# Optimization experiments

Measured on AMD Instinct MI355X. Metric: run time of the kernel, lower is better.

## Reference

```python
import jax, jax.numpy as jnp
import numpy as np
from jax import lax

H = 32   # hidden_size
L = 8    # num_layers
D_IN = 64    # lstm input_size / fc0 out
FEAT = 4096  # feature_size
T = 300      # frame_size
B = 64       # batch


def setup_inputs() -> dict:
    key = jax.random.key(0)
    ks = jax.random.split(key, 16)
    s = 0.05
    inp = {
        "x": jax.random.normal(ks[0], (B, T, FEAT), dtype=jnp.float32),
        # fc0: Linear(4096->64), ReLU, Dropout(eval), Linear(64->64)
        "W0": jax.random.normal(ks[1], (D_IN, FEAT), dtype=jnp.float32) * s,
        "b0": jax.random.normal(ks[2], (D_IN,), dtype=jnp.float32) * s,
        "W1": jax.random.normal(ks[3], (D_IN, D_IN), dtype=jnp.float32) * s,
        "b1": jax.random.normal(ks[4], (D_IN,), dtype=jnp.float32) * s,
        # LSTM params, PyTorch layout: W_ih [4H, in], W_hh [4H, H], biases [4H]
        "Wih0": jax.random.normal(ks[5], (4 * H, D_IN), dtype=jnp.float32) * s,
        "Wih": jax.random.normal(ks[6], (L - 1, 4 * H, H), dtype=jnp.float32) * s,
        "Whh": jax.random.normal(ks[7], (L, 4 * H, H), dtype=jnp.float32) * s,
        "bih": jax.random.normal(ks[8], (L, 4 * H), dtype=jnp.float32) * s,
        "bhh": jax.random.normal(ks[9], (L, 4 * H), dtype=jnp.float32) * s,
        # fc1: 32 -> 1 ; fc2: 300 -> 1
        "Wfc1": jax.random.normal(ks[10], (1, H), dtype=jnp.float32) * s,
        "bfc1": jax.random.normal(ks[11], (1,), dtype=jnp.float32) * s,
        "Wfc2": jax.random.normal(ks[12], (1, T), dtype=jnp.float32) * s,
        "bfc2": jax.random.normal(ks[13], (1,), dtype=jnp.float32) * s,
    }
    return inp


def _lstm_layer(x_seq, Wih_l, Whh_l, bih_l, bhh_l):
    # x_seq: [B, T, in] -> h_seq: [B, T, H]; PyTorch gate order i,f,g,o
    gx = jnp.einsum('bti,gi->btg', x_seq, Wih_l) + bih_l  # [B,T,4H]
    b = x_seq.shape[0]
    init = (jnp.zeros((b, H), x_seq.dtype), jnp.zeros((b, H), x_seq.dtype))

    def step(carry, gx_t):
        h, c = carry
        g = gx_t + h @ Whh_l.T + bhh_l
        i, f, gg, o = jnp.split(g, 4, axis=-1)
        c = jax.nn.sigmoid(f) * c + jax.nn.sigmoid(i) * jnp.tanh(gg)
        h = jax.nn.sigmoid(o) * jnp.tanh(c)
        return (h, c), h

    _, hs = lax.scan(step, init, jnp.swapaxes(gx, 0, 1))  # hs: [T,B,H]
    return jnp.swapaxes(hs, 0, 1)


def reference(x, W0, b0, W1, b1, Wih0, Wih, Whh, bih, bhh, Wfc1, bfc1, Wfc2, bfc2):
    # fc0 (dropout is identity in eval mode)
    h = jax.nn.relu(jnp.einsum('btf,of->bto', x, W0) + b0)
    h = jnp.einsum('bti,oi->bto', h, W1) + b1  # [B,T,64]
    # stacked LSTM, h0=c0=0
    for l in range(L):
        Wih_l = Wih0 if l == 0 else Wih[l - 1]
        h = _lstm_layer(h, Wih_l, Whh[l], bih[l], bhh[l])  # [B,T,32]
    # fc1 over hidden, squeeze, fc2 over time, squeeze
    y = jnp.einsum('bth,oh->bto', h, Wfc1)[..., 0] + bfc1[0]  # [B,T]
    y = y @ Wfc2.T + bfc2  # [B,1]
    return y[:, 0]
```

## Files before the change

kernel.cpp:

```cpp
#include <hip/hip_runtime.h>
#include <cstdint>

#define FEAT 4096
#define DIN  64
#define HS   32
#define NL   8
#define TT   300
#define BB   64
#define G4   128
#define MROWS (BB*TT)
#define KS    4
#define KSLICE (FEAT/KS)
#define BK    64
#define NCHUNK (KSLICE/BK)

typedef __bf16 bf16x8 __attribute__((ext_vector_type(8)));
typedef float  f32x4  __attribute__((ext_vector_type(4)));
typedef unsigned short u16x8 __attribute__((ext_vector_type(8)));

__device__ __forceinline__ float sigm(float x){ return __fdividef(1.f, 1.f + __expf(-x)); }
__device__ __forceinline__ float tanh_f(float x){ return __fdividef(2.f, 1.f + __expf(-2.f*x)) - 1.f; }

__device__ __forceinline__ unsigned short bf16_rne(float f){
    uint32_t u = __float_as_uint(f);
    return (unsigned short)((u + 0x7FFFu + ((u >> 16) & 1u)) >> 16);
}

__global__ __launch_bounds__(256) void w0split(const float* __restrict__ W0,
                                               unsigned short* __restrict__ wh,
                                               unsigned short* __restrict__ wl)
{
    const int i = (blockIdx.x * 256 + threadIdx.x) * 4;
    float4 v = *(const float4*)(W0 + i);
    float f[4] = {v.x, v.y, v.z, v.w};
    unsigned short hh[4], ll[4];
    #pragma unroll
    for (int j = 0; j < 4; ++j) {
        unsigned short h = bf16_rne(f[j]);
        float fh = __uint_as_float((uint32_t)h << 16);
        hh[j] = h;
        ll[j] = bf16_rne(f[j] - fh);
    }
    *(ushort4*)(wh + i) = make_ushort4(hh[0], hh[1], hh[2], hh[3]);
    *(ushort4*)(wl + i) = make_ushort4(ll[0], ll[1], ll[2], ll[3]);
}

__global__ __launch_bounds__(256, 2) void fc_gemm1(
    const float* __restrict__ x,
    const unsigned short* __restrict__ wh,
    const unsigned short* __restrict__ wl,
    float* __restrict__ part)
{
    __shared__ __align__(16) unsigned short xh[2][64][64];
    __shared__ __align__(16) unsigned short xl[2][64][64];
    __shared__ __align__(16) unsigned short wh_s[2][64][64];
    __shared__ __align__(16) unsigned short wl_s[2][64][64];

    const int t   = threadIdx.x;
    const int l   = t & 63;
    const int w   = t >> 6;
    const int rbb = (w >> 1) * 32;
    const int cbb = (w & 1) * 32;
    const int r0  = blockIdx.x * 64;
    const int kb0 = blockIdx.y * KSLICE;

    const int srow = t >> 3;
    const int sg   = t & 7;

    f32x4 acc[2][2];
    #pragma unroll
    for (int i = 0; i < 2; ++i)
        #pragma unroll
        for (int j = 0; j < 2; ++j)
            acc[i][j] = (f32x4){0.f, 0.f, 0.f, 0.f};

    float4 xr[2][2];
    uint4  w0h[2], w0l[2];

    auto LOAD = [&](int c) {
        const float* xb = x + (size_t)r0 * FEAT + kb0 + c * BK;
        xr[0][0] = *(const float4*)(xb + (size_t)srow * FEAT + sg * 8);
        xr[0][1] = *(const float4*)(xb + (size_t)srow * FEAT + sg * 8 + 4);
        xr[1][0] = *(const float4*)(xb + (size_t)(srow + 32) * FEAT + sg * 8);
        xr[1][1] = *(const float4*)(xb + (size_t)(srow + 32) * FEAT + sg * 8 + 4);
        const int wo = kb0 + c * BK + sg * 8;
        w0h[0] = *(const uint4*)(wh + (size_t)srow * FEAT + wo);
        w0h[1] = *(const uint4*)(wh + (size_t)(srow + 32) * FEAT + wo);
        w0l[0] = *(const uint4*)(wl + (size_t)srow * FEAT + wo);
        w0l[1] = *(const uint4*)(wl + (size_t)(srow + 32) * FEAT + wo);
    };

    auto STORE = [&](int c) {
        const int buf = c & 1;
        #pragma unroll
        for (int j = 0; j < 2; ++j) {
            const int row = srow + j * 32;
            const int gsw = (sg ^ (row & 7)) * 8;
            float f0[8] = {xr[j][0].x, xr[j][0].y, xr[j][0].z, xr[j][0].w,
                           xr[j][1].x, xr[j][1].y, xr[j][1].z, xr[j][1].w};
            u16x8 vh, vl;
            #pragma unroll
            for (int i = 0; i < 8; ++i) {
                const __bf16 bh = (__bf16)f0[i];
                const float  fh = (float)bh;
                const __bf16 bl = (__bf16)(f0[i] - fh);
                vh[i] = __builtin_bit_cast(unsigned short, bh);
                vl[i] = __builtin_bit_cast(unsigned short, bl);
            }
            *(u16x8*)&xh[buf][row][gsw] = vh;
            *(u16x8*)&xl[buf][row][gsw] = vl;
            *(uint4*)&wh_s[buf][row][gsw] = w0h[j];
            *(uint4*)&wl_s[buf][row][gsw] = w0l[j];
        }
    };

    auto COMPUTE = [&](int buf) {
        #pragma unroll
        for (int kstep = 0; kstep < 2; ++kstep) {
            const int gA = kstep * 4 + (l >> 4);
            bf16x8 Ah[2], Al[2], Bh[2], Bl[2];
            #pragma unroll
            for (int rf = 0; rf < 2; ++rf) {
                const int ra  = rbb + rf * 16 + (l & 15);
                const int off = (gA ^ (ra & 7)) * 8;
                Ah[rf] = __builtin_bit_cast(bf16x8, *(const u16x8*)&xh[buf][ra][off]);
                Al[rf] = __builtin_bit_cast(bf16x8, *(const u16x8*)&xl[buf][ra][off]);
            }
            #pragma unroll
            for (int cf = 0; cf < 2; ++cf) {
                const int cb  = cbb + cf * 16 + (l & 15);
                const int off = (gA ^ (cb & 7)) * 8;
                Bh[cf] = __builtin_bit_cast(bf16x8, *(const u16x8*)&wh_s[buf][cb][off]);
                Bl[cf] = __builtin_bit_cast(bf16x8, *(const u16x8*)&wl_s[buf][cb][off]);
            }
            #pragma unroll
            for (int rf = 0; rf < 2; ++rf)
                #pragma unroll
                for (int cf = 0; cf < 2; ++cf) {
                    acc[rf][cf] = __builtin_amdgcn_mfma_f32_16x16x32_bf16(Ah[rf], Bh[cf], acc[rf][cf], 0, 0, 0);
                    acc[rf][cf] = __builtin_amdgcn_mfma_f32_16x16x32_bf16(Al[rf], Bh[cf], acc[rf][cf], 0, 0, 0);
                    acc[rf][cf] = __builtin_amdgcn_mfma_f32_16x16x32_bf16(Ah[rf], Bl[cf], acc[rf][cf], 0, 0, 0);
                }
        }
    };

    LOAD(0);
    for (int c = 0; c < NCHUNK; ++c) {
        STORE(c);
        if (c + 1 < NCHUNK) LOAD(c + 1);
        asm volatile("s_waitcnt lgkmcnt(0)" ::: "memory");
        __builtin_amdgcn_s_barrier();
        COMPUTE(c & 1);
    }

    #pragma unroll
    for (int rf = 0; rf < 2; ++rf)
        #pragma unroll
        for (int cf = 0; cf < 2; ++cf)
            #pragma unroll
            for (int r = 0; r < 4; ++r) {
                const int row = r0 + rbb + rf * 16 + (l >> 4) * 4 + r;
                const int col = cbb + cf * 16 + (l & 15);
                part[((size_t)blockIdx.y * MROWS + row) * 64 + col] = acc[rf][cf][r];
            }
}

__global__ __launch_bounds__(256) void fc_tail(
    const float* __restrict__ part, const float* __restrict__ b0,
    const float* __restrict__ W1, const float* __restrict__ b1,
    const float* __restrict__ Wih0,
    const float* __restrict__ bih, const float* __restrict__ bhh,
    float* __restrict__ gx0)
{
    __shared__ __align__(16) float h1s[64][68];
    __shared__ __align__(16) float h2s[64][68];

    const int tid = threadIdx.x;
    const int tc  = tid & 15;
    const int tr  = tid >> 4;
    const int r0  = blockIdx.x * 64;

    {
        const int row = tid >> 2;
        const int c0  = (tid & 3) * 16;
        float4 s[4];
        #pragma unroll
        for (int i = 0; i < 4; ++i)
            s[i] = *(const float4*)(part + ((size_t)(r0 + row)) * 64 + c0 + 4 * i);
        #pragma unroll
        for (int ks = 1; ks < KS; ++ks)
            #pragma unroll
            for (int i = 0; i < 4; ++i) {
                float4 v = *(const float4*)(part + ((size_t)ks * MROWS + r0 + row) * 64 + c0 + 4 * i);
                s[i].x += v.x; s[i].y += v.y; s[i].z += v.z; s[i].w += v.w;
            }
        #pragma unroll
        for (int i = 0; i < 4; ++i) {
            float4 bv = *(const float4*)(b0 + c0 + 4 * i);
            float4 o;
            o.x = fmaxf(s[i].x + bv.x, 0.f);
            o.y = fmaxf(s[i].y + bv.y, 0.f);
            o.z = fmaxf(s[i].z + bv.z, 0.f);
            o.w = fmaxf(s[i].w + bv.w, 0.f);
            *(float4*)&h1s[row][c0 + 4 * i] = o;
        }
    }
    __syncthreads();

    float acc2[4][4] = {};
    #pragma unroll
    for (int k4 = 0; k4 < 16; ++k4) {
        const int k = k4 * 4;
        float4 a[4], wv[4];
        #pragma unroll
        for (int i = 0; i < 4; ++i) a[i] = *(const float4*)&h1s[tr * 4 + i][k];
        #pragma unroll
        for (int j = 0; j < 4; ++j) wv[j] = *(const float4*)(W1 + (size_t)(tc * 4 + j) * DIN + k);
        #pragma unroll
        for (int i = 0; i < 4; ++i)
            #pragma unroll
            for (int j = 0; j < 4; ++j)
                acc2[i][j] += a[i].x * wv[j].x + a[i].y * wv[j].y + a[i].z * wv[j].z + a[i].w * wv[j].w;
    }
    __syncthreads();
    #pragma unroll
    for (int i = 0; i < 4; ++i)
        #pragma unroll
        for (int j = 0; j < 4; ++j)
            h2s[tr * 4 + i][tc * 4 + j] = acc2[i][j] + b1[tc * 4 + j];
    __syncthreads();

    #pragma unroll
    for (int p = 0; p < 2; ++p) {
        float acc3[4][4] = {};
        #pragma unroll
        for (int k4 = 0; k4 < 16; ++k4) {
            const int k = k4 * 4;
            float4 a[4], wv[4];
            #pragma unroll
            for (int i = 0; i < 4; ++i) a[i] = *(const float4*)&h2s[tr * 4 + i][k];
            #pragma unroll
            for (int j = 0; j < 4; ++j) wv[j] = *(const float4*)(Wih0 + (size_t)(p * 64 + tc * 4 + j) * DIN + k);
            #pragma unroll
            for (int i = 0; i < 4; ++i)
                #pragma unroll
                for (int j = 0; j < 4; ++j)
                    acc3[i][j] += a[i].x * wv[j].x + a[i].y * wv[j].y + a[i].z * wv[j].z + a[i].w * wv[j].w;
        }
        const int g0 = p * 64 + tc * 4;
        #pragma unroll
        for (int i = 0; i < 4; ++i) {
            float4 ov;
            ov.x = acc3[i][0] + bih[g0 + 0] + bhh[g0 + 0];
            ov.y = acc3[i][1] + bih[g0 + 1] + bhh[g0 + 1];
            ov.z = acc3[i][2] + bih[g0 + 2] + bhh[g0 + 2];
            ov.w = acc3[i][3] + bih[g0 + 3] + bhh[g0 + 3];
            *(float4*)(gx0 + (size_t)(r0 + tr * 4 + i) * G4 + g0) = ov;
        }
    }
}

__global__ __launch_bounds__(512, 2) void lstm_all(
    const float* __restrict__ gx0,
    const float* __restrict__ Wih, const float* __restrict__ Whh,
    const float* __restrict__ bih, const float* __restrict__ bhh,
    const float* __restrict__ Wfc1, const float* __restrict__ bfc1,
    const float* __restrict__ Wfc2, const float* __restrict__ bfc2,
    float* __restrict__ out)
{
    const int b    = blockIdx.x;
    const int tid  = threadIdx.x;
    const int l    = tid >> 6;
    const int lane = tid & 63;
    const int q0   = lane;
    const int q1   = lane + 64;

    __shared__ __align__(16) float hbuf[NL][2][HS];
    __shared__ __align__(16) float gbuf[NL][G4];
    __shared__ __align__(16) float h7[TT][HS];
    __shared__ float red[NL];

    float whh0[HS], whh1[HS], wih0[HS], wih1[HS];
    {
        const float* whhl = Whh + (size_t)l * G4 * HS;
        const float* wihl = Wih + (size_t)(l > 0 ? l - 1 : 0) * G4 * HS;
        #pragma unroll
        for (int k4 = 0; k4 < 8; ++k4) {
            float4 v0 = *(const float4*)(whhl + q0 * HS + 4 * k4);
            float4 v1 = *(const float4*)(whhl + q1 * HS + 4 * k4);
            whh0[4*k4+0]=v0.x; whh0[4*k4+1]=v0.y; whh0[4*k4+2]=v0.z; whh0[4*k4+3]=v0.w;
            whh1[4*k4+0]=v1.x; whh1[4*k4+1]=v1.y; whh1[4*k4+2]=v1.z; whh1[4*k4+3]=v1.w;
            float4 u0 = *(const float4*)(wihl + q0 * HS + 4 * k4);
            float4 u1 = *(const float4*)(wihl + q1 * HS + 4 * k4);
            wih0[4*k4+0]=u0.x; wih0[4*k4+1]=u0.y; wih0[4*k4+2]=u0.z; wih0[4*k4+3]=u0.w;
            wih1[4*k4+0]=u1.x; wih1[4*k4+1]=u1.y; wih1[4*k4+2]=u1.z; wih1[4*k4+3]=u1.w;
        }
    }
    const float bias0 = (l > 0) ? (bih[l*G4 + q0] + bhh[l*G4 + q0]) : 0.f;
    const float bias1 = (l > 0) ? (bih[l*G4 + q1] + bhh[l*G4 + q1]) : 0.f;

    float c_state = 0.f;

    const float* gxb = gx0 + (size_t)b * TT * G4;
    float pf0 = 0.f, pf1 = 0.f;
    if (l == 0) { pf0 = gxb[q0]; pf1 = gxb[q1]; }

    for (int s = 0; s < TT + NL - 1; ++s) {
        const int t = s - l;
        if (0 <= t && t < TT) {
            float acc0, acc1;
            if (l == 0) {
                acc0 = pf0; acc1 = pf1;
                const int tn = t + 1;
                if (tn < TT) { pf0 = gxb[(size_t)tn * G4 + q0]; pf1 = gxb[(size_t)tn * G4 + q1]; }
            } else {
                acc0 = bias0; acc1 = bias1;
            }
            float a0a = 0.f, a0b = 0.f, a1a = 0.f, a1b = 0.f;
            if (t > 0) {
                const float4* hp = (const float4*)hbuf[l][(t - 1) & 1];
                #pragma unroll
                for (int k4 = 0; k4 < 8; ++k4) {
                    float4 v = hp[k4];
                    a0a = fmaf(whh0[4*k4+0], v.x, a0a); a0b = fmaf(whh0[4*k4+1], v.y, a0b);
                    a0a = fmaf(whh0[4*k4+2], v.z, a0a); a0b = fmaf(whh0[4*k4+3], v.w, a0b);
                    a1a = fmaf(whh1[4*k4+0], v.x, a1a); a1b = fmaf(whh1[4*k4+1], v.y, a1b);
                    a1a = fmaf(whh1[4*k4+2], v.z, a1a); a1b = fmaf(whh1[4*k4+3], v.w, a1b);
                }
            }
            if (l > 0) {
                const float4* hq = (const float4*)hbuf[l - 1][t & 1];
                #pragma unroll
                for (int k4 = 0; k4 < 8; ++k4) {
                    float4 v = hq[k4];
                    a0a = fmaf(wih0[4*k4+0], v.x, a0a); a0b = fmaf(wih0[4*k4+1], v.y, a0b);
                    a0a = fmaf(wih0[4*k4+2], v.z, a0a); a0b = fmaf(wih0[4*k4+3], v.w, a0b);
                    a1a = fmaf(wih1[4*k4+0], v.x, a1a); a1b = fmaf(wih1[4*k4+1], v.y, a1b);
                    a1a = fmaf(wih1[4*k4+2], v.z, a1a); a1b = fmaf(wih1[4*k4+3], v.w, a1b);
                }
            }
            acc0 += a0a + a0b;
            acc1 += a1a + a1b;
            gbuf[l][q0] = acc0;
            gbuf[l][q1] = acc1;
            asm volatile("s_waitcnt lgkmcnt(0)" ::: "memory");
            if (lane < HS) {
                const float ig = gbuf[l][lane];
                const float fg = gbuf[l][HS + lane];
                const float gg = gbuf[l][2*HS + lane];
                const float og = gbuf[l][3*HS + lane];
                c_state = sigm(fg) * c_state + sigm(ig) * tanh_f(gg);
                const float hv = sigm(og) * tanh_f(c_state);
                hbuf[l][t & 1][lane] = hv;
                if (l == NL - 1) h7[t][lane] = hv;
            }
        }
        __syncthreads();
    }

    float part = 0.f;
    for (int t = tid; t < TT; t += 512) {
        float st = 0.f;
        #pragma unroll
        for (int j = 0; j < HS; ++j) st = fmaf(h7[t][j], Wfc1[j], st);
        part += (st + bfc1[0]) * Wfc2[t];
    }
    #pragma unroll
    for (int off = 32; off >= 1; off >>= 1) part += __shfl_down(part, off, 64);
    if (lane == 0) red[l] = part;
    __syncthreads();
    if (tid == 0) {
        float tot = 0.f;
        #pragma unroll
        for (int w = 0; w < NL; ++w) tot += red[w];
        out[b] = tot + bfc2[0];
    }
}

extern "C" void kernel_launch(void* const* d_in, const int* in_sizes, int n_in,
                              void* d_out, int out_size, void* d_ws, size_t ws_size,
                              hipStream_t stream) {
    const float* x    = (const float*)d_in[0];
    const float* W0   = (const float*)d_in[1];
    const float* b0   = (const float*)d_in[2];
    const float* W1   = (const float*)d_in[3];
    const float* b1   = (const float*)d_in[4];
    const float* Wih0 = (const float*)d_in[5];
    const float* Wih  = (const float*)d_in[6];
    const float* Whh  = (const float*)d_in[7];
    const float* bih  = (const float*)d_in[8];
    const float* bhh  = (const float*)d_in[9];
    const float* Wfc1 = (const float*)d_in[10];
    const float* bfc1 = (const float*)d_in[11];
    const float* Wfc2 = (const float*)d_in[12];
    const float* bfc2 = (const float*)d_in[13];

    char* wsb = (char*)d_ws;
    float*          gx0 = (float*)wsb;
    unsigned short* wh  = (unsigned short*)(wsb + 9830400);
    unsigned short* wl  = (unsigned short*)(wsb + 9830400 + 524288);
    float*          prt = (float*)(wsb + 9830400 + 1048576);

    w0split <<<256, 256, 0, stream>>>(W0, wh, wl);
    fc_gemm1<<<dim3(MROWS / 64, KS), 256, 0, stream>>>(x, wh, wl, prt);
    fc_tail <<<MROWS / 64, 256, 0, stream>>>(prt, b0, W1, b1, Wih0, bih, bhh, gx0);
    lstm_all<<<BB, 512, 0, stream>>>(gx0, Wih, Whh, bih, bhh, Wfc1, bfc1, Wfc2, bfc2,
                                     (float*)d_out);
}
```

Before: 438.0 us.

## Use readlane broadcasts and lane shuffles in LSTM step; double-buffer fc0 loads

Each LSTM layer wavefront now keeps its hidden state in registers. It broadcasts h via readlane for the recurrent matvec and exchanges gate pre-activations with a xor-32 shuffle, so gates no longer round-trip through the shared gbuf array and its LDS wait. Lanes are remapped so each half-wave holds the i/f or g/o gates for the same hidden unit, and both halves compute the cell update redundantly. Separately, the fc0 GEMM loop is unrolled by two with A/B register sets, so global loads are issued two chunks ahead. This costs more registers and relies on NCHUNK being even.

Result: slower. 524.9 us (+19.9%).

```diff
diff --git a/kernel.cpp b/kernel.cpp
--- a/kernel.cpp
+++ b/kernel.cpp
@@ -21,6 +21,10 @@
 __device__ __forceinline__ float sigm(float x){ return __fdividef(1.f, 1.f + __expf(-x)); }
 __device__ __forceinline__ float tanh_f(float x){ return __fdividef(2.f, 1.f + __expf(-2.f*x)) - 1.f; }
 
+__device__ __forceinline__ float rdlane(float v, int k){
+    return __builtin_bit_cast(float, __builtin_amdgcn_readlane(__builtin_bit_cast(int, v), k));
+}
+
 __device__ __forceinline__ unsigned short bf16_rne(float f){
     uint32_t u = __float_as_uint(f);
     return (unsigned short)((u + 0x7FFFu + ((u >> 16) & 1u)) >> 16);
@@ -74,24 +78,35 @@
         for (int j = 0; j < 2; ++j)
             acc[i][j] = (f32x4){0.f, 0.f, 0.f, 0.f};
 
-    float4 xr[2][2];
-    uint4  w0h[2], w0l[2];
-
-    auto LOAD = [&](int c) {
+    float4 xrA[2][2], xrB[2][2];
+    uint4  whA[2], wlA[2], whB[2], wlB[2];
+
+    auto LOADA = [&](int c) {
         const float* xb = x + (size_t)r0 * FEAT + kb0 + c * BK;
-        xr[0][0] = *(const float4*)(xb + (size_t)srow * FEAT + sg * 8);
-        xr[0][1] = *(const float4*)(xb + (size_t)srow * FEAT + sg * 8 + 4);
-        xr[1][0] = *(const float4*)(xb + (size_t)(srow + 32) * FEAT + sg * 8);
-        xr[1][1] = *(const float4*)(xb + (size_t)(srow + 32) * FEAT + sg * 8 + 4);
+        xrA[0][0] = *(const float4*)(xb + (size_t)srow * FEAT + sg * 8);
+        xrA[0][1] = *(const float4*)(xb + (size_t)srow * FEAT + sg * 8 + 4);
+        xrA[1][0] = *(const float4*)(xb + (size_t)(srow + 32) * FEAT + sg * 8);
+        xrA[1][1] = *(const float4*)(xb + (size_t)(srow + 32) * FEAT + sg * 8 + 4);
         const int wo = kb0 + c * BK + sg * 8;
-        w0h[0] = *(const uint4*)(wh + (size_t)srow * FEAT + wo);
-        w0h[1] = *(const uint4*)(wh + (size_t)(srow + 32) * FEAT + wo);
-        w0l[0] = *(const uint4*)(wl + (size_t)srow * FEAT + wo);
-        w0l[1] = *(const uint4*)(wl + (size_t)(srow + 32) * FEAT + wo);
+        whA[0] = *(const uint4*)(wh + (size_t)srow * FEAT + wo);
+        whA[1] = *(const uint4*)(wh + (size_t)(srow + 32) * FEAT + wo);
+        wlA[0] = *(const uint4*)(wl + (size_t)srow * FEAT + wo);
+        wlA[1] = *(const uint4*)(wl + (size_t)(srow + 32) * FEAT + wo);
     };
-
-    auto STORE = [&](int c) {
-        const int buf = c & 1;
+    auto LOADB = [&](int c) {
+        const float* xb = x + (size_t)r0 * FEAT + kb0 + c * BK;
+        xrB[0][0] = *(const float4*)(xb + (size_t)srow * FEAT + sg * 8);
+        xrB[0][1] = *(const float4*)(xb + (size_t)srow * FEAT + sg * 8 + 4);
+        xrB[1][0] = *(const float4*)(xb + (size_t)(srow + 32) * FEAT + sg * 8);
+        xrB[1][1] = *(const float4*)(xb + (size_t)(srow + 32) * FEAT + sg * 8 + 4);
+        const int wo = kb0 + c * BK + sg * 8;
+        whB[0] = *(const uint4*)(wh + (size_t)srow * FEAT + wo);
+        whB[1] = *(const uint4*)(wh + (size_t)(srow + 32) * FEAT + wo);
+        wlB[0] = *(const uint4*)(wl + (size_t)srow * FEAT + wo);
+        wlB[1] = *(const uint4*)(wl + (size_t)(srow + 32) * FEAT + wo);
+    };
+
+    auto STOREIMPL = [&](int buf, float4 (&xr)[2][2], uint4 (&w0h)[2], uint4 (&w0l)[2]) {
         #pragma unroll
         for (int j = 0; j < 2; ++j) {
             const int row = srow + j * 32;
@@ -144,13 +159,19 @@
         }
     };
 
-    LOAD(0);
-    for (int c = 0; c < NCHUNK; ++c) {
-        STORE(c);
-        if (c + 1 < NCHUNK) LOAD(c + 1);
+    LOADA(0);
+    LOADB(1);
+    for (int c = 0; c < NCHUNK; c += 2) {
+        STOREIMPL(0, xrA, whA, wlA);
+        if (c + 2 < NCHUNK) LOADA(c + 2);
         asm volatile("s_waitcnt lgkmcnt(0)" ::: "memory");
         __builtin_amdgcn_s_barrier();
-        COMPUTE(c & 1);
+        COMPUTE(0);
+        STOREIMPL(1, xrB, whB, wlB);
+        if (c + 3 < NCHUNK) LOADB(c + 3);
+        asm volatile("s_waitcnt lgkmcnt(0)" ::: "memory");
+        __builtin_amdgcn_s_barrier();
+        COMPUTE(1);
     }
 
     #pragma unroll
@@ -272,11 +293,12 @@
     const int tid  = threadIdx.x;
     const int l    = tid >> 6;
     const int lane = tid & 63;
-    const int q0   = lane;
-    const int q1   = lane + 64;
+    const int m    = lane & 31;
+    const int half = lane >> 5;
+    const int q0   = half * 64 + m;
+    const int q1   = q0 + 32;
 
     __shared__ __align__(16) float hbuf[NL][2][HS];
-    __shared__ __align__(16) float gbuf[NL][G4];
     __shared__ __align__(16) float h7[TT][HS];
     __shared__ float red[NL];
 
@@ -300,6 +322,7 @@
     const float bias1 = (l > 0) ? (bih[l*G4 + q1] + bhh[l*G4 + q1]) : 0.f;
 
     float c_state = 0.f;
+    float hv = 0.f;
 
     const float* gxb = gx0 + (size_t)b * TT * G4;
     float pf0 = 0.f, pf1 = 0.f;
@@ -316,41 +339,45 @@
             } else {
                 acc0 = bias0; acc1 = bias1;
             }
+
             float a0a = 0.f, a0b = 0.f, a1a = 0.f, a1b = 0.f;
             if (t > 0) {
-                const float4* hp = (const float4*)hbuf[l][(t - 1) & 1];
                 #pragma unroll
-                for (int k4 = 0; k4 < 8; ++k4) {
-                    float4 v = hp[k4];
-                    a0a = fmaf(whh0[4*k4+0], v.x, a0a); a0b = fmaf(whh0[4*k4+1], v.y, a0b);
-                    a0a = fmaf(whh0[4*k4+2], v.z, a0a); a0b = fmaf(whh0[4*k4+3], v.w, a0b);
-                    a1a = fmaf(whh1[4*k4+0], v.x, a1a); a1b = fmaf(whh1[4*k4+1], v.y, a1b);
-                    a1a = fmaf(whh1[4*k4+2], v.z, a1a); a1b = fmaf(whh1[4*k4+3], v.w, a1b);
+                for (int k = 0; k < HS; k += 2) {
+                    const float hk0 = rdlane(hv, k);
+                    const float hk1 = rdlane(hv, k + 1);
+                    a0a = fmaf(hk0, whh0[k],   a0a);
+                    a0b = fmaf(hk1, whh0[k+1], a0b);
+                    a1a = fmaf(hk0, whh1[k],   a1a);
+                    a1b = fmaf(hk1, whh1[k+1], a1b);
                 }
             }
             if (l > 0) {
-                const float4* hq = (const float4*)hbuf[l - 1][t & 1];
+                const float hx = hbuf[l - 1][t & 1][m];
                 #pragma unroll
-                for (int k4 = 0; k4 < 8; ++k4) {
-                    float4 v = hq[k4];
-                    a0a = fmaf(wih0[4*k4+0], v.x, a0a); a0b = fmaf(wih0[4*k4+1], v.y, a0b);
-                    a0a = fmaf(wih0[4*k4+2], v.z, a0a); a0b = fmaf(wih0[4*k4+3], v.w, a0b);
-                    a1a = fmaf(wih1[4*k4+0], v.x, a1a); a1b = fmaf(wih1[4*k4+1], v.y, a1b);
-                    a1a = fmaf(wih1[4*k4+2], v.z, a1a); a1b = fmaf(wih1[4*k4+3], v.w, a1b);
+                for (int k = 0; k < HS; k += 2) {
+                    const float hk0 = rdlane(hx, k);
+                    const float hk1 = rdlane(hx, k + 1);
+                    a0a = fmaf(hk0, wih0[k],   a0a);
+                    a0b = fmaf(hk1, wih0[k+1], a0b);
+                    a1a = fmaf(hk0, wih1[k],   a1a);
+                    a1b = fmaf(hk1, wih1[k+1], a1b);
                 }
             }
             acc0 += a0a + a0b;
             acc1 += a1a + a1b;
-            gbuf[l][q0] = acc0;
-            gbuf[l][q1] = acc1;
-            asm volatile("s_waitcnt lgkmcnt(0)" ::: "memory");
+
+            const float sw0 = __shfl_xor(acc0, 32, 64);
+            const float sw1 = __shfl_xor(acc1, 32, 64);
+            const float gi = half ? sw0  : acc0;
+            const float gf = half ? sw1  : acc1;
+            const float gg = half ? acc0 : sw0;
+            const float go = half ? acc1 : sw1;
+
+            c_state = sigm(gf) * c_state + sigm(gi) * tanh_f(gg);
+            hv = sigm(go) * tanh_f(c_state);
+
             if (lane < HS) {
-                const float ig = gbuf[l][lane];
-                const float fg = gbuf[l][HS + lane];
-                const float gg = gbuf[l][2*HS + lane];
-                const float og = gbuf[l][3*HS + lane];
-                c_state = sigm(fg) * c_state + sigm(ig) * tanh_f(gg);
-                const float hv = sigm(og) * tanh_f(c_state);
                 hbuf[l][t & 1][lane] = hv;
                 if (l == NL - 1) h7[t][lane] = hv;
             }
```
